# Performance work log

Measured on AMD Instinct MI355X. Metric: run time of the kernel, lower is better.

The kernel has to match this reference:

```python
import jax, jax.numpy as jnp
import numpy as np

B, S, K, N, G = 4, 16, 8192, 8192, 128
NUM_GROUPS = K // G

def setup_inputs() -> dict:
    key = jax.random.key(0)
    k1, k2, k3, k4, k5 = jax.random.split(key, 5)
    x = jax.random.normal(k1, (B, S, K), dtype=jnp.float32)
    qweight = jax.random.randint(k2, (K, N), -128, 128, dtype=jnp.int32)
    # small positive scales like real quantizers produce
    scales = jax.random.uniform(k3, (NUM_GROUPS, N), dtype=jnp.float32) * 0.01 + 1e-4
    zeros = jax.random.uniform(k4, (NUM_GROUPS, N), dtype=jnp.float32) * 2.0 - 1.0
    bias = jax.random.normal(k5, (N,), dtype=jnp.float32)
    return {"x": x, "qweight": qweight, "scales": scales, "zeros": zeros,
            "bias": bias, "group_size": G}

def reference(x, qweight, scales, zeros, bias, group_size):
    # Expand per-group scale/zero along K: [num_groups, N] -> [K, N]
    Kdim = qweight.shape[0]
    if scales.shape[0] == 1:
        scale_exp = jnp.broadcast_to(scales, (Kdim, scales.shape[1]))
        zero_exp = jnp.broadcast_to(zeros, (Kdim, zeros.shape[1]))
    else:
        scale_exp = jnp.repeat(scales, group_size, axis=0)[:Kdim]
        zero_exp = jnp.repeat(zeros, group_size, axis=0)[:Kdim]
    # Dequantize: W[k, n] = (q - zero) * scale
    weight_fp = (qweight.astype(x.dtype) - zero_exp) * scale_exp  # [K, N]
    out = jnp.einsum('bsk,kn->bsn', x, weight_fp) + bias
    return out
```

## Files before the change

kernel.cpp:

```cpp
#include <hip/hip_runtime.h>

typedef __attribute__((ext_vector_type(8))) short short8;
typedef __attribute__((ext_vector_type(8))) unsigned short ushort8;
typedef __attribute__((ext_vector_type(4))) unsigned short ushort4v;
typedef __attribute__((ext_vector_type(4))) int int4v;
typedef __attribute__((ext_vector_type(4))) float f32x4;

#define Mdim 64
#define Kdim 8192
#define Ndim 8192
#define GRP 128
#define NGRP 64
#define KSPLIT 4
#define NG2 (NGRP / KSPLIT)
#define BN 128

#define SWZ(row, kk) ((row)*128 + ((kk) ^ (8*((((row) >> 3) ^ (row)) & 7))))

__device__ __forceinline__ unsigned short f2bf(float f) {
    unsigned int u = __builtin_bit_cast(unsigned int, f);
    u += 0x7FFFu + ((u >> 16) & 1u);
    return (unsigned short)(u >> 16);
}
__device__ __forceinline__ float bf2f(unsigned short h) {
    unsigned int u = ((unsigned int)h) << 16;
    return __builtin_bit_cast(float, u);
}

__global__ void prep_kernel(const float* __restrict__ x,
                            unsigned short* __restrict__ xh,
                            unsigned short* __restrict__ xl,
                            float* __restrict__ xsum) {
    const int tid = threadIdx.x;
    const int u = blockIdx.x * 8 + (tid >> 5);
    const int g = u & (NGRP - 1);
    const int m = u >> 6;
    const int lane = tid & 31;
    const int k = g * GRP + lane * 4;
    f32x4 v = *(const f32x4*)(x + (size_t)m * Kdim + k);
    ushort4v hv, lv;
    float s = 0.f;
#pragma unroll
    for (int i = 0; i < 4; ++i) {
        unsigned short h = f2bf(v[i]);
        hv[i] = h;
        lv[i] = f2bf(v[i] - bf2f(h));
        s += v[i];
    }
    *(ushort4v*)(xh + (size_t)m * Kdim + k) = hv;
    *(ushort4v*)(xl + (size_t)m * Kdim + k) = lv;
#pragma unroll
    for (int off = 16; off > 0; off >>= 1) s += __shfl_down(s, off, 32);
    if (lane == 0) xsum[g * Mdim + m] = s;
}

__launch_bounds__(512)
__global__ void qlin_kernel(const unsigned short* __restrict__ xh,
                            const unsigned short* __restrict__ xl,
                            const int* __restrict__ qw,
                            const float* __restrict__ scales,
                            const float* __restrict__ zeros,
                            const float* __restrict__ xsum,
                            float* __restrict__ pout) {
    __shared__ unsigned short lq[2][128 * 128];
    __shared__ unsigned short lxh[64 * 128];
    __shared__ unsigned short lxl[64 * 128];

    const int tid = threadIdx.x;
    const int kh = blockIdx.x & (KSPLIT - 1);
    const int n0 = (blockIdx.x >> 2) * BN;
    const int g0 = kh * NG2;

    const int w = tid >> 6;
    const int l = tid & 63;
    const int lcol = l & 15;
    const int lhi = l >> 4;

    const int qc = tid & 31;
    const int qr = tid >> 5;
    const int xc = tid & 15;
    const int xm = tid >> 4;

    const int nn = n0 + w * 16 + lcol;

    int4v qv[8];
    ushort8 xga, xgb, xgc, xgd;
    float s_n, z_n, s_c, z_c;
    f32x4 xs_n[4], xs_c[4];

    auto LOAD_SZX = [&](int g) {
        s_n = scales[(size_t)g * Ndim + nn];
        z_n = zeros[(size_t)g * Ndim + nn];
#pragma unroll
        for (int mf = 0; mf < 4; ++mf)
            xs_n[mf] = *(const f32x4*)(xsum + g * Mdim + mf * 16 + lhi * 4);
    };
    auto LOADX = [&](int g) {
        const size_t kb = (size_t)g * GRP + xc * 8;
        xga = *(const ushort8*)(xh + (size_t)xm * Kdim + kb);
        xgb = *(const ushort8*)(xh + (size_t)(xm + 32) * Kdim + kb);
        xgc = *(const ushort8*)(xl + (size_t)xm * Kdim + kb);
        xgd = *(const ushort8*)(xl + (size_t)(xm + 32) * Kdim + kb);
    };
    auto LOADQ = [&](int g) {
        const size_t kb = (size_t)g * GRP + qr * 8;
        const int nc = n0 + qc * 4;
#pragma unroll
        for (int j = 0; j < 8; ++j)
            qv[j] = *(const int4v*)(qw + (kb + j) * Ndim + nc);
    };
    auto WRITEX = [&]() {
        *(ushort8*)&lxh[SWZ(xm, xc * 8)] = xga;
        *(ushort8*)&lxh[SWZ(xm + 32, xc * 8)] = xgb;
        *(ushort8*)&lxl[SWZ(xm, xc * 8)] = xgc;
        *(ushort8*)&lxl[SWZ(xm + 32, xc * 8)] = xgd;
    };
    auto WRITEQ = [&](int bb) {
#pragma unroll
        for (int i = 0; i < 4; ++i) {
            int4v pk;
#pragma unroll
            for (int t = 0; t < 4; ++t) {
                unsigned lo = __builtin_bit_cast(unsigned, (float)qv[2 * t][i]) >> 16;
                unsigned hi = __builtin_bit_cast(unsigned, (float)qv[2 * t + 1][i]) & 0xFFFF0000u;
                pk[t] = (int)(lo | hi);
            }
            *(int4v*)&lq[bb][SWZ(qc * 4 + i, qr * 8)] = pk;
        }
    };

    f32x4 acc[4];
#pragma unroll
    for (int mf = 0; mf < 4; ++mf) acc[mf] = {0.f, 0.f, 0.f, 0.f};

    LOAD_SZX(g0);
    LOADX(g0);
    LOADQ(g0);
    s_c = s_n; z_c = z_n;
#pragma unroll
    for (int mf = 0; mf < 4; ++mf) xs_c[mf] = xs_n[mf];
    WRITEX();
    WRITEQ(0);
    __syncthreads();

    for (int g = 0; g < NG2; ++g) {
        const int bb = g & 1;
        const bool more = (g + 1 < NG2);

        if (more) {
            LOAD_SZX(g0 + g + 1);
            LOADX(g0 + g + 1);
            LOADQ(g0 + g + 1);
        }

        short8 bq[4];
#pragma unroll
        for (int ks = 0; ks < 4; ++ks)
            bq[ks] = *(const short8*)&lq[bb][SWZ(w * 16 + lcol, ks * 32 + lhi * 8)];
#pragma unroll
        for (int mf = 0; mf < 4; ++mf) {
            short8 ah[4], al[4];
#pragma unroll
            for (int ks = 0; ks < 4; ++ks) {
                ah[ks] = *(const short8*)&lxh[SWZ(mf * 16 + lcol, ks * 32 + lhi * 8)];
                al[ks] = *(const short8*)&lxl[SWZ(mf * 16 + lcol, ks * 32 + lhi * 8)];
            }
            f32x4 p = {0.f, 0.f, 0.f, 0.f};
#pragma unroll
            for (int ks = 0; ks < 4; ++ks) {
                p = __builtin_amdgcn_mfma_f32_16x16x32_bf16(ah[ks], bq[ks], p, 0, 0, 0);
                p = __builtin_amdgcn_mfma_f32_16x16x32_bf16(al[ks], bq[ks], p, 0, 0, 0);
            }
#pragma unroll
            for (int r = 0; r < 4; ++r)
                acc[mf][r] += s_c * (p[r] - z_c * xs_c[mf][r]);
        }

        if (more) {
            __syncthreads();
            s_c = s_n; z_c = z_n;
#pragma unroll
            for (int mf = 0; mf < 4; ++mf) xs_c[mf] = xs_n[mf];
            WRITEX();
            WRITEQ(bb ^ 1);
            __syncthreads();
        }
    }

    const size_t ob = (size_t)kh * Mdim * Ndim;
#pragma unroll
    for (int mf = 0; mf < 4; ++mf)
#pragma unroll
        for (int r = 0; r < 4; ++r)
            pout[ob + (size_t)(mf * 16 + lhi * 4 + r) * Ndim + nn] = acc[mf][r];
}

__global__ void reduce_kernel(const float* __restrict__ pout,
                              const float* __restrict__ bias,
                              float* __restrict__ out) {
    const size_t e = ((size_t)blockIdx.x * 256 + threadIdx.x) * 4;
    const int n = (int)(e & (Ndim - 1));
    f32x4 a = *(const f32x4*)(bias + n);
#pragma unroll
    for (int s = 0; s < KSPLIT; ++s) {
        f32x4 ppart = *(const f32x4*)(pout + (size_t)s * Mdim * Ndim + e);
#pragma unroll
        for (int r = 0; r < 4; ++r) a[r] += ppart[r];
    }
    *(f32x4*)(out + e) = a;
}

extern "C" void kernel_launch(void* const* d_in, const int* in_sizes, int n_in,
                              void* d_out, int out_size, void* d_ws, size_t ws_size,
                              hipStream_t stream) {
    const float* x = (const float*)d_in[0];
    const int* qw = (const int*)d_in[1];
    const float* scales = (const float*)d_in[2];
    const float* zeros = (const float*)d_in[3];
    const float* bias = (const float*)d_in[4];

    unsigned short* xh = (unsigned short*)d_ws;
    unsigned short* xl = xh + (size_t)Mdim * Kdim;
    float* xsum = (float*)(xl + (size_t)Mdim * Kdim);
    float* pout = xsum + NGRP * Mdim;
    float* out = (float*)d_out;

    prep_kernel<<<512, 256, 0, stream>>>(x, xh, xl, xsum);
    qlin_kernel<<<(Ndim / BN) * KSPLIT, 512, 0, stream>>>(xh, xl, qw, scales, zeros, xsum, pout);
    reduce_kernel<<<(Mdim * Ndim / 4) / 256, 256, 0, stream>>>(pout, bias, out);
}
```

Measured before the change: 66.15 us.

## Prefetch quantized weights two groups ahead with double register buffers

Deepens the global-load pipeline for the int32 weight tile so it is fetched two K-groups ahead into alternating register arrays, while scales and x stay one group ahead. This gives the weight loads, the dominant memory traffic, more time in flight before they are converted and written to LDS. It also adds a min-blocks-per-CU hint of 2 to launch_bounds. The extra 8 int4 registers per thread compete with that occupancy hint and may cause spills or limit waves.

New measurement: 79.20 us. 1.2x slower.

```diff
diff --git a/kernel.cpp b/kernel.cpp
--- a/kernel.cpp
+++ b/kernel.cpp
@@ -54,7 +54,29 @@
     if (lane == 0) xsum[g * Mdim + m] = s;
 }
 
-__launch_bounds__(512)
+#define LOADQ_M(dst, g) do {                                                  \
+    const size_t kb_ = (size_t)(g) * GRP + qr * 8;                            \
+    const int nc_ = n0 + qc * 4;                                              \
+    _Pragma("unroll")                                                         \
+    for (int j = 0; j < 8; ++j)                                               \
+        dst[j] = *(const int4v*)(qw + (kb_ + j) * Ndim + nc_);                \
+} while (0)
+
+#define WRITEQ_M(src, bb) do {                                                \
+    _Pragma("unroll")                                                         \
+    for (int i = 0; i < 4; ++i) {                                             \
+        int4v pk_;                                                            \
+        _Pragma("unroll")                                                     \
+        for (int t = 0; t < 4; ++t) {                                         \
+            unsigned lo_ = __builtin_bit_cast(unsigned, (float)src[2*t][i]) >> 16;        \
+            unsigned hi_ = __builtin_bit_cast(unsigned, (float)src[2*t+1][i]) & 0xFFFF0000u; \
+            pk_[t] = (int)(lo_ | hi_);                                        \
+        }                                                                     \
+        *(int4v*)&lq[bb][SWZ(qc * 4 + i, qr * 8)] = pk_;                      \
+    }                                                                         \
+} while (0)
+
+__launch_bounds__(512, 2)
 __global__ void qlin_kernel(const unsigned short* __restrict__ xh,
                             const unsigned short* __restrict__ xl,
                             const int* __restrict__ qw,
@@ -83,7 +105,7 @@
 
     const int nn = n0 + w * 16 + lcol;
 
-    int4v qv[8];
+    int4v qva[8], qvb[8];
     ushort8 xga, xgb, xgc, xgd;
     float s_n, z_n, s_c, z_c;
     f32x4 xs_n[4], xs_c[4];
@@ -102,57 +124,19 @@
         xgc = *(const ushort8*)(xl + (size_t)xm * Kdim + kb);
         xgd = *(const ushort8*)(xl + (size_t)(xm + 32) * Kdim + kb);
     };
-    auto LOADQ = [&](int g) {
-        const size_t kb = (size_t)g * GRP + qr * 8;
-        const int nc = n0 + qc * 4;
-#pragma unroll
-        for (int j = 0; j < 8; ++j)
-            qv[j] = *(const int4v*)(qw + (kb + j) * Ndim + nc);
-    };
     auto WRITEX = [&]() {
         *(ushort8*)&lxh[SWZ(xm, xc * 8)] = xga;
         *(ushort8*)&lxh[SWZ(xm + 32, xc * 8)] = xgb;
         *(ushort8*)&lxl[SWZ(xm, xc * 8)] = xgc;
         *(ushort8*)&lxl[SWZ(xm + 32, xc * 8)] = xgd;
     };
-    auto WRITEQ = [&](int bb) {
-#pragma unroll
-        for (int i = 0; i < 4; ++i) {
-            int4v pk;
-#pragma unroll
-            for (int t = 0; t < 4; ++t) {
-                unsigned lo = __builtin_bit_cast(unsigned, (float)qv[2 * t][i]) >> 16;
-                unsigned hi = __builtin_bit_cast(unsigned, (float)qv[2 * t + 1][i]) & 0xFFFF0000u;
-                pk[t] = (int)(lo | hi);
-            }
-            *(int4v*)&lq[bb][SWZ(qc * 4 + i, qr * 8)] = pk;
-        }
-    };
 
     f32x4 acc[4];
 #pragma unroll
     for (int mf = 0; mf < 4; ++mf) acc[mf] = {0.f, 0.f, 0.f, 0.f};
 
-    LOAD_SZX(g0);
-    LOADX(g0);
-    LOADQ(g0);
-    s_c = s_n; z_c = z_n;
-#pragma unroll
-    for (int mf = 0; mf < 4; ++mf) xs_c[mf] = xs_n[mf];
-    WRITEX();
-    WRITEQ(0);
-    __syncthreads();
-
-    for (int g = 0; g < NG2; ++g) {
+    auto COMPUTE = [&](int g) {
         const int bb = g & 1;
-        const bool more = (g + 1 < NG2);
-
-        if (more) {
-            LOAD_SZX(g0 + g + 1);
-            LOADX(g0 + g + 1);
-            LOADQ(g0 + g + 1);
-        }
-
         short8 bq[4];
 #pragma unroll
         for (int ks = 0; ks < 4; ++ks)
@@ -175,17 +159,42 @@
             for (int r = 0; r < 4; ++r)
                 acc[mf][r] += s_c * (p[r] - z_c * xs_c[mf][r]);
         }
-
-        if (more) {
-            __syncthreads();
-            s_c = s_n; z_c = z_n;
-#pragma unroll
-            for (int mf = 0; mf < 4; ++mf) xs_c[mf] = xs_n[mf];
-            WRITEX();
-            WRITEQ(bb ^ 1);
-            __syncthreads();
-        }
+    };
+
+    LOAD_SZX(g0);
+    LOADX(g0);
+    LOADQ_M(qva, g0);
+    s_c = s_n; z_c = z_n;
+#pragma unroll
+    for (int mf = 0; mf < 4; ++mf) xs_c[mf] = xs_n[mf];
+    WRITEX();
+    WRITEQ_M(qva, 0);
+    LOADQ_M(qva, g0 + 1);
+    __syncthreads();
+
+#define STEP(G, CUR, NXT) do {                                                \
+    const int g_ = (G);                                                       \
+    const bool m1_ = (g_ + 1 < NG2);                                          \
+    const bool m2_ = (g_ + 2 < NG2);                                          \
+    if (m1_) { LOAD_SZX(g0 + g_ + 1); LOADX(g0 + g_ + 1); }                   \
+    if (m2_) LOADQ_M(NXT, g0 + g_ + 2);                                       \
+    COMPUTE(g_);                                                              \
+    if (m1_) {                                                                \
+        __syncthreads();                                                      \
+        s_c = s_n; z_c = z_n;                                                 \
+        _Pragma("unroll")                                                     \
+        for (int mf = 0; mf < 4; ++mf) xs_c[mf] = xs_n[mf];                   \
+        WRITEX();                                                             \
+        WRITEQ_M(CUR, (g_ + 1) & 1);                                          \
+        __syncthreads();                                                      \
+    }                                                                         \
+} while (0)
+
+    for (int gg = 0; gg < NG2; gg += 2) {
+        STEP(gg, qva, qvb);
+        STEP(gg + 1, qvb, qva);
     }
+#undef STEP
 
     const size_t ob = (size_t)kh * Mdim * Ndim;
 #pragma unroll
```
